# Optimization experiments

Measured on AMD Instinct MI355X. Metric: run time of the kernel, lower is better.

The kernel has to match this reference:

```python
import jax, jax.numpy as jnp
import numpy as np

T_, B_, C_ = 1, 2, 4
D_, H_, W_ = 32, 32, 32
RES = (16, 16, 16)          # (Dlat, Hlat, Wlat)
K_ = 32                      # fixed max neighbors (pad+mask)
RADIUS = 0.055
OUT_CH = 128
NUM_CH = 32                  # pos-embedding channels per coord
MAXP = 10000.0
EMB = 3 * NUM_CH             # 96


def _pos_embed(coords):
    # transformer sinusoidal embedding: [..., 3] -> [..., 96]
    freq = 1.0 / (MAXP ** (jnp.arange(0, NUM_CH, 2, dtype=jnp.float32) / NUM_CH))  # [16]
    ang = coords[..., None] * freq                                   # [..., 3, 16]
    emb = jnp.concatenate([jnp.sin(ang), jnp.cos(ang)], axis=-1)     # [..., 3, 32]
    return emb.reshape(coords.shape[:-1] + (EMB,))


def _kernel_mlp(h, W0, b0, W1, b1, W2, b2, W3, b3):
    # LinearChannelMLP layers [196,128,256,128,128] with gelu between layers
    h = jax.nn.gelu(h @ W0 + b0)
    h = jax.nn.gelu(h @ W1 + b1)
    h = jax.nn.gelu(h @ W2 + b2)
    return h @ W3 + b3


def _make_input_grid():
    # grid_coords[b] has shape [H, W, D, 3]; flatten matches f_y's (h w d) order
    th = np.linspace(0.0, 1.0, H_, dtype=np.float32)
    tw = np.linspace(0.0, 1.0, W_, dtype=np.float32)
    td = np.linspace(0.0, 1.0, D_, dtype=np.float32)
    Xh, Yw, Zd = np.meshgrid(th, tw, td, indexing='ij')
    return np.stack([Xh, Yw, Zd], axis=-1)  # [H, W, D, 3]


def _make_latent_grid():
    # mirrors __init__: tx over res[1], ty over res[2], tz over res[0]
    tx = np.linspace(0.0, 1.0, RES[1], dtype=np.float32)
    ty = np.linspace(0.0, 1.0, RES[2], dtype=np.float32)
    tz = np.linspace(0.0, 1.0, RES[0], dtype=np.float32)
    X, Y, Z = np.meshgrid(tx, ty, tz, indexing='ij')
    return np.stack([X, Y, Z], axis=-1).reshape(-1, 3)  # [Nq, 3]


def _radius_neighbors(q, y, radius, k):
    # brute-force KDTree replacement: k nearest within radius, padded + masked
    nq = q.shape[0]
    idx = np.zeros((nq, k), np.int32)
    msk = np.zeros((nq, k), bool)
    r2 = radius * radius
    for s in range(0, nq, 512):
        qb = q[s:s + 512]
        d2 = ((qb[:, None, :] - y[None, :, :]) ** 2).sum(-1)  # [chunk, Ny]
        part = np.argpartition(d2, k, axis=1)[:, :k]
        pd = np.take_along_axis(d2, part, 1)
        order = np.argsort(pd, axis=1)
        part = np.take_along_axis(part, order, 1)
        pd = np.take_along_axis(pd, order, 1)
        idx[s:s + 512] = part.astype(np.int32)
        msk[s:s + 512] = pd <= r2
    return idx, msk


def setup_inputs() -> dict:
    key = jax.random.key(0)
    ks = jax.random.split(key, 9)
    x = jax.random.normal(ks[0], (T_, B_, C_, D_, H_, W_), jnp.float32)

    gc = _make_input_grid()                                   # [H,W,D,3]
    grid_coords = jnp.asarray(np.broadcast_to(gc, (B_,) + gc.shape).copy())
    lat = _make_latent_grid()                                 # [Nq,3]
    latent_grid = jnp.asarray(lat)

    # bbox of grid is [0,1]^3 so rescaled latent grid == latent_grid here
    idx, msk = _radius_neighbors(lat, gc.reshape(-1, 3), RADIUS, K_)
    nbr_idx = jnp.asarray(np.broadcast_to(idx, (B_,) + idx.shape).copy())
    nbr_mask = jnp.asarray(np.broadcast_to(msk, (B_,) + msk.shape).copy())

    kin = 2 * EMB + C_  # 196
    def lin(k, fin, fout):
        return jax.random.normal(k, (fin, fout), jnp.float32) / np.float32(np.sqrt(fin))
    W0 = lin(ks[1], kin, 128); b0 = jnp.zeros((128,), jnp.float32)
    W1 = lin(ks[2], 128, 256); b1 = jnp.zeros((256,), jnp.float32)
    W2 = lin(ks[3], 256, 128); b2 = jnp.zeros((128,), jnp.float32)
    W3 = lin(ks[4], 128, OUT_CH); b3 = jnp.zeros((OUT_CH,), jnp.float32)

    return {"x": x, "grid_coords": grid_coords, "latent_grid": latent_grid,
            "nbr_idx": nbr_idx, "nbr_mask": nbr_mask,
            "W0": W0, "b0": b0, "W1": W1, "b1": b1,
            "W2": W2, "b2": b2, "W3": W3, "b3": b3}


def reference(x, grid_coords, latent_grid, nbr_idx, nbr_mask,
              W0, b0, W1, b1, W2, b2, W3, b3):
    T, B, C, D, H, W = x.shape
    Dl, Hl, Wl = RES
    # 't b c d h w -> b t (h w d) c'
    f = jnp.transpose(x, (1, 0, 4, 5, 3, 2)).reshape(B, T, H * W * D, C)
    y = grid_coords.reshape(B, -1, 3)                         # [B,Ny,3]
    bmin = y.min(axis=1, keepdims=True)
    bmax = y.max(axis=1, keepdims=True)
    lat = bmin + (bmax - bmin) * latent_grid[None]            # [B,Nq,3]

    y_emb = _pos_embed(y)                                     # [B,Ny,96]
    x_emb = _pos_embed(lat)                                   # [B,Nq,96]

    def per_batch(y_e, x_e, f_b, idx, msk):
        # gather neighbor features (ragged -> padded fixed-K)
        rep = y_e[idx]                                        # [Nq,K,96]
        slf = jnp.broadcast_to(x_e[:, None, :], rep.shape)    # [Nq,K,96]
        f_nbr = f_b[:, idx]                                   # [T,Nq,K,C]
        coord_feat = jnp.concatenate([rep, slf], axis=-1)     # [Nq,K,192]
        agg = jnp.concatenate(
            [jnp.broadcast_to(coord_feat[None], (f_b.shape[0],) + coord_feat.shape),
             f_nbr], axis=-1)                                 # [T,Nq,K,196]
        k = _kernel_mlp(agg, W0, b0, W1, b1, W2, b2, W3, b3)  # [T,Nq,K,out]
        k = k * msk[None, :, :, None].astype(k.dtype)
        return k.sum(axis=2)                                  # [T,Nq,out] (reduction='sum')

    out = jax.vmap(per_batch)(y_emb, x_emb, f, nbr_idx, nbr_mask)  # [B,T,Nq,out]
    # 'b t (h w d) c -> t b c d h w'
    out = out.reshape(B, T, Hl, Wl, Dl, -1)
    out = jnp.transpose(out, (1, 0, 5, 4, 2, 3))              # [T,B,out,Dl,Hl,Wl]
    return out
```

## Files before the change

### kernel.cpp

```cpp
#include <hip/hip_runtime.h>
#include <hip/hip_bf16.h>
#include <math.h>


typedef short bs8 __attribute__((ext_vector_type(8)));
typedef float f4  __attribute__((ext_vector_type(4)));
typedef float f2  __attribute__((ext_vector_type(2)));

#define MFMA16 __builtin_amdgcn_mfma_f32_16x16x32_bf16

#define W1T_OFF    0u
#define W2T_OFF    65536u
#define W3T_OFF    131072u
#define W0ET_OFF   163840u
#define W0MT_OFF   188416u
#define VQ_OFF     212992u
#define GF_OFF     2310144u
#define ST_OFF     19087360u
#define CNT_OFF    23281664u
#define FAST_NEED  23314432u

#define OW0AT_OFF   0
#define OW1T_OFF    32768
#define OW2T_OFF    98304
#define OW3T_OFF    163840
#define OSTAGED_OFF 196608
#define OLD_NEED    (196608 + 4194304)

__device__ __forceinline__ short f2bf(float f) {
  unsigned u = __float_as_uint(f);
  return (short)((u + 0x7FFFu + ((u >> 16) & 1u)) >> 16);
}
__device__ __forceinline__ float bf2f(short s) {
  return __uint_as_float(((unsigned)(unsigned short)s) << 16);
}
__device__ __forceinline__ unsigned pk2bf(float lo, float hi) {
  __hip_bfloat162 h = __float22bfloat162_rn(float2{lo, hi});
  return *reinterpret_cast<unsigned*>(&h);
}
__device__ __forceinline__ f2 gelu2(f2 x) {
  f2 t = x * x;
  f2 z = x * (t * 0.10294322f + 2.3022077f);
  f2 e;
  e.x = __builtin_exp2f(z.x);
  e.y = __builtin_exp2f(z.y);
  f2 d = e + 1.0f;
  f2 r;
  r.x = __builtin_amdgcn_rcpf(d.x);
  r.y = __builtin_amdgcn_rcpf(d.y);
  return x - x * r;
}
__device__ __forceinline__ float gelu_old(float x) {
  float z = 0.7978845608028654f * fmaf(0.044715f * x, x * x, x);
  float e = __expf(2.0f * z);
  return 0.5f * x * (2.0f - 2.0f / (e + 1.0f));
}


__global__ void gno_prep3(const float* __restrict__ W0, const float* __restrict__ W1,
                          const float* __restrict__ W2, const float* __restrict__ W3,
                          short* __restrict__ W1T, short* __restrict__ W2T,
                          short* __restrict__ W3T, short* __restrict__ W0eT,
                          short* __restrict__ W0mT) {
  int g = blockIdx.x * 256 + threadIdx.x;
  if (g < 32768) {
    int nn = g >> 7, k = g & 127;
    W1T[g] = f2bf(W1[k * 256 + nn]);
  } else if (g < 65536) {
    int h = g - 32768, nn = h >> 8, k = h & 255;
    W2T[h] = f2bf(W2[k * 128 + nn]);
  } else if (g < 81920) {
    int h = g - 65536, nn = h >> 7, k = h & 127;
    W3T[h] = f2bf(W3[k * 128 + nn]);
  } else if (g < 94208) {
    int h = g - 81920, nn = h / 96, k = h % 96;
    W0eT[h] = f2bf(W0[k * 128 + nn]);
  } else if (g < 106496) {
    int h = g - 94208, nn = h / 96, k = h % 96;
    W0mT[h] = f2bf(W0[(96 + k) * 128 + nn]);
  }
}

__global__ __launch_bounds__(256, 4) void gno_gfvq(
    const float* __restrict__ x, const float* __restrict__ gc,
    const float* __restrict__ latg, const float* __restrict__ W0,
    const float* __restrict__ b0,
    const short* __restrict__ W0eT, const short* __restrict__ W0mT,
    short* __restrict__ GF, float* __restrict__ vqPre) {
  __shared__ __align__(16) short embS[64 * 104];
  __shared__ __align__(16) short tileS[64 * 132];
  __shared__ float gcS[192];
  __shared__ float xS[2][4][64];
  __shared__ float wfS[4][128];
  __shared__ float freqS[16];

  const int tid = threadIdx.x;
  const int blk = blockIdx.x;
  const bool isGF = blk < 512;
  const int p0 = isGF ? blk * 64 : (blk - 512) * 64;

  if (tid < 16) freqS[tid] = (float)exp(-(double)tid * (9.210340371976184 / 16.0));
  if (tid < 192) gcS[tid] = isGF ? gc[p0 * 3 + tid] : latg[p0 * 3 + tid];
  if (isGF) {
#pragma unroll
    for (int u = 0; u < 2; ++u) {
      int slot = tid * 2 + u;
      int bb = slot >> 8, ch = (slot >> 6) & 3, i = slot & 63;
      int n = p0 + i;
      xS[bb][ch][i] = x[((bb * 4 + ch) << 15) + ((n & 31) << 10) + (n >> 5)];
      wfS[slot >> 7][slot & 127] = W0[(192 + (slot >> 7)) * 128 + (slot & 127)];
    }
  }
  __syncthreads();
  {
    int rr = tid >> 2, c4 = tid & 3;
#pragma unroll
    for (int c = c4 * 24; c < c4 * 24 + 24; ++c) {
      int a = c >> 5, jj = c & 31;
      float v = (jj < 16) ? __sinf(gcS[rr * 3 + a] * freqS[jj])
                          : __cosf(gcS[rr * 3 + a] * freqS[jj & 15]);
      embS[rr * 104 + c] = f2bf(v);
    }
  }
  __syncthreads();
  const int wid = tid >> 6, lane = tid & 63;
  const int l15 = lane & 15, lg = lane >> 4;
  const int f0 = wid * 32;
  const short* WT = isGF ? W0eT : W0mT;
  f4 acc[2][4] = {};
#pragma unroll
  for (int ks = 0; ks < 3; ++ks) {
    bs8 Aw[2], Be[4];
#pragma unroll
    for (int ft = 0; ft < 2; ++ft)
      Aw[ft] = *(const bs8*)(WT + (f0 + ft * 16 + l15) * 96 + ks * 32 + lg * 8);
#pragma unroll
    for (int pt = 0; pt < 4; ++pt)
      Be[pt] = *(const bs8*)(embS + (pt * 16 + l15) * 104 + ks * 32 + lg * 8);
#pragma unroll
    for (int ft = 0; ft < 2; ++ft)
#pragma unroll
      for (int pt = 0; pt < 4; ++pt)
        acc[ft][pt] = MFMA16(Aw[ft], Be[pt], acc[ft][pt], 0, 0, 0);
  }
  if (!isGF) {
#pragma unroll
    for (int ft = 0; ft < 2; ++ft) {
      f4 bias = *(const f4*)(b0 + f0 + ft * 16 + lg * 4);
#pragma unroll
      for (int pt = 0; pt < 4; ++pt) {
        int q = p0 + pt * 16 + l15;
        *(f4*)(vqPre + q * 128 + f0 + ft * 16 + lg * 4) = acc[ft][pt] + bias;
      }
    }
    return;
  }
#pragma unroll 1
  for (int bb = 0; bb < 2; ++bb) {
#pragma unroll
    for (int ft = 0; ft < 2; ++ft) {
      f4 wf0 = *(const f4*)(&wfS[0][f0 + ft * 16 + lg * 4]);
      f4 wf1 = *(const f4*)(&wfS[1][f0 + ft * 16 + lg * 4]);
      f4 wf2 = *(const f4*)(&wfS[2][f0 + ft * 16 + lg * 4]);
      f4 wf3 = *(const f4*)(&wfS[3][f0 + ft * 16 + lg * 4]);
#pragma unroll
      for (int pt = 0; pt < 4; ++pt) {
        int p = pt * 16 + l15;
        float x0 = xS[bb][0][p], x1 = xS[bb][1][p], x2 = xS[bb][2][p], x3 = xS[bb][3][p];
        float v0 = acc[ft][pt][0] + x0 * wf0[0] + x1 * wf1[0] + x2 * wf2[0] + x3 * wf3[0];
        float v1 = acc[ft][pt][1] + x0 * wf0[1] + x1 * wf1[1] + x2 * wf2[1] + x3 * wf3[1];
        float v2 = acc[ft][pt][2] + x0 * wf0[2] + x1 * wf1[2] + x2 * wf2[2] + x3 * wf3[2];
        float v3 = acc[ft][pt][3] + x0 * wf0[3] + x1 * wf1[3] + x2 * wf2[3] + x3 * wf3[3];
        uint2 pp;
        pp.x = pk2bf(v0, v1);
        pp.y = pk2bf(v2, v3);
        *(uint2*)(tileS + p * 132 + f0 + ft * 16 + lg * 4) = pp;
      }
    }
    __syncthreads();
    {
      int row = tid >> 2, c4 = tid & 3;
      const short* src = tileS + row * 132 + c4 * 32;
      short* dst = GF + ((size_t)((bb << 15) + p0 + row)) * 128 + c4 * 32;
      *(uint4*)(dst)      = *(const uint4*)(src);
      *(uint4*)(dst + 8)  = *(const uint4*)(src + 8);
      *(uint4*)(dst + 16) = *(const uint4*)(src + 16);
      *(uint4*)(dst + 24) = *(const uint4*)(src + 24);
    }
    __syncthreads();
  }
}

__device__ __forceinline__ uint4 gelu8u(uint4 gu, const float* vrow) {
  uint4 r;
  const unsigned ua[4] = {gu.x, gu.y, gu.z, gu.w};
  unsigned ro[4];
#pragma unroll
  for (int j = 0; j < 4; ++j) {
    f2 xx;
    xx.x = __uint_as_float(ua[j] << 16);
    xx.y = __uint_as_float(ua[j] & 0xFFFF0000u);
    xx += *(const f2*)(vrow + 2 * j);
    f2 g = gelu2(xx);
    ro[j] = pk2bf(g.x, g.y);
  }
  r.x = ro[0]; r.y = ro[1]; r.z = ro[2]; r.w = ro[3];
  return r;
}

__global__ __launch_bounds__(256, 4) void gno_main5(
    const float* __restrict__ gc, const float* __restrict__ latg,
    const int* __restrict__ nidx,
    const float* __restrict__ b1, const float* __restrict__ b2,
    const short* __restrict__ W1T, const short* __restrict__ W2T,
    const float* __restrict__ vqPre, const short* __restrict__ GF,
    float* __restrict__ staged, float* __restrict__ cntG) {
  __shared__ __align__(16) short h0S[64][136];
  __shared__ __align__(16) short h1S[64][136];
  __shared__ float vqS[2][128];
  __shared__ float maskfS[64];

  const int tid = threadIdx.x;
  const int blk = blockIdx.x;
  const int b = blk >> 11;
  const int q0 = (blk & 2047) * 2;

  vqS[tid >> 7][tid & 127] = vqPre[(q0 + (tid >> 7)) * 128 + (tid & 127)];

  const int r = tid >> 2, seg = tid & 3;
  const int qh = r >> 5;
  const int n = nidx[(q0 + qh) * 32 + (r & 31)];
  const uint4* gp = (const uint4*)(GF + ((size_t)((b << 15) + n)) * 128 + seg * 32);
  uint4 g0 = gp[0], g1 = gp[1], g2 = gp[2], g3 = gp[3];
  if (seg == 0) {
    float la = latg[(q0 + qh) * 3], lb = latg[(q0 + qh) * 3 + 1], lc = latg[(q0 + qh) * 3 + 2];
    float d0 = __fsub_rn(la, gc[n * 3]);
    float d1 = __fsub_rn(lb, gc[n * 3 + 1]);
    float d2 = __fsub_rn(lc, gc[n * 3 + 2]);
    float s = __fadd_rn(__fadd_rn(__fmul_rn(d0, d0), __fmul_rn(d1, d1)), __fmul_rn(d2, d2));
    maskfS[r] = ((double)s <= 0.055 * 0.055) ? 1.0f : 0.0f;
  }
  __syncthreads();
  {
    const float* vrow = vqS[qh] + seg * 32;
    *(uint4*)(&h0S[r][seg * 32]) = gelu8u(g0, vrow);
    *(uint4*)(&h0S[r][seg * 32 + 8]) = gelu8u(g1, vrow + 8);
    *(uint4*)(&h0S[r][seg * 32 + 16]) = gelu8u(g2, vrow + 16);
    *(uint4*)(&h0S[r][seg * 32 + 24]) = gelu8u(g3, vrow + 24);
  }
  __syncthreads();
  if (tid < 2) {
    float s = 0.0f;
#pragma unroll
    for (int i = 0; i < 32; ++i) s += maskfS[tid * 32 + i];
    cntG[(b << 12) + q0 + tid] = s;
  }

  const int wid = tid >> 6, lane = tid & 63;
  const int l15 = lane & 15, lg = lane >> 4;
  const int mh = wid >> 1, nh = wid & 1;
  f4 accL2[4][2] = {};

#pragma unroll 1
  for (int c = 0; c < 2; ++c) {
    {
      const int f0l = wid * 32;
      const int fg = c * 128 + f0l;
      f4 acc[2][4] = {};
#pragma unroll
      for (int ks = 0; ks < 4; ++ks) {
        bs8 Aw[2], Bh[4];
#pragma unroll
        for (int ft = 0; ft < 2; ++ft)
          Aw[ft] = *(const bs8*)(W1T + (fg + ft * 16 + l15) * 128 + ks * 32 + lg * 8);
#pragma unroll
        for (int rt = 0; rt < 4; ++rt)
          Bh[rt] = *(const bs8*)(&h0S[rt * 16 + l15][ks * 32 + lg * 8]);
#pragma unroll
        for (int ft = 0; ft < 2; ++ft)
#pragma unroll
          for (int rt = 0; rt < 4; ++rt)
            acc[ft][rt] = MFMA16(Aw[ft], Bh[rt], acc[ft][rt], 0, 0, 0);
      }
#pragma unroll
      for (int ft = 0; ft < 2; ++ft) {
        f4 bias = *(const f4*)(b1 + fg + ft * 16 + lg * 4);
#pragma unroll
        for (int rt = 0; rt < 4; ++rt) {
          f2 a = {acc[ft][rt][0] + bias[0], acc[ft][rt][1] + bias[1]};
          f2 bpair = {acc[ft][rt][2] + bias[2], acc[ft][rt][3] + bias[3]};
          f2 ga = gelu2(a);
          f2 gb = gelu2(bpair);
          uint2 p;
          p.x = pk2bf(ga.x, ga.y);
          p.y = pk2bf(gb.x, gb.y);
          *(uint2*)(&h1S[rt * 16 + l15][f0l + ft * 16 + lg * 4]) = p;
        }
      }
    }
    __syncthreads();
    {
      const int fo = nh * 64;
#pragma unroll
      for (int ks = 0; ks < 4; ++ks) {
        bs8 Ah[2], Bw[4];
#pragma unroll
        for (int rt = 0; rt < 2; ++rt)
          Ah[rt] = *(const bs8*)(&h1S[mh * 32 + rt * 16 + l15][ks * 32 + lg * 8]);
#pragma unroll
        for (int ct = 0; ct < 4; ++ct)
          Bw[ct] = *(const bs8*)(W2T + (fo + ct * 16 + l15) * 256 + c * 128 + ks * 32 + lg * 8);
#pragma unroll
        for (int ct = 0; ct < 4; ++ct)
#pragma unroll
          for (int rt = 0; rt < 2; ++rt)
            accL2[ct][rt] = MFMA16(Ah[rt], Bw[ct], accL2[ct][rt], 0, 0, 0);
      }
    }
    __syncthreads();
  }

  {
    const int fo = nh * 64;
    float psum[4];
#pragma unroll
    for (int ct = 0; ct < 4; ++ct) {
      float bias = b2[fo + ct * 16 + l15];
      float s = 0.0f;
#pragma unroll
      for (int rt = 0; rt < 2; ++rt) {
        f2 u0 = {accL2[ct][rt][0] + bias, accL2[ct][rt][1] + bias};
        f2 u1 = {accL2[ct][rt][2] + bias, accL2[ct][rt][3] + bias};
        f2 gA = gelu2(u0);
        f2 gB = gelu2(u1);
        int row = mh * 32 + rt * 16 + lg * 4;
        s += gA.x * maskfS[row] + gA.y * maskfS[row + 1] +
             gB.x * maskfS[row + 2] + gB.y * maskfS[row + 3];
      }
      psum[ct] = s;
    }
#pragma unroll
    for (int ct = 0; ct < 4; ++ct) {
      psum[ct] += __shfl_xor(psum[ct], 16, 64);
      psum[ct] += __shfl_xor(psum[ct], 32, 64);
    }
    if (lane < 16) {
      float* op = staged + ((size_t)((b << 12) + q0 + mh)) * 128 + fo;
      op[lane] = psum[0];
      op[16 + lane] = psum[1];
      op[32 + lane] = psum[2];
      op[48 + lane] = psum[3];
    }
  }
}

__global__ __launch_bounds__(256, 2) void gno_fin2(
    const float* __restrict__ staged, const float* __restrict__ cntG,
    const short* __restrict__ W3T, const float* __restrict__ b3,
    float* __restrict__ out) {
  __shared__ __align__(16) float tileS[16 * 260];
  __shared__ float cntS[256];
  __shared__ float b3S[128];
  const int tid = threadIdx.x, blk = blockIdx.x;
  const int b = blk >> 5;
  const int hi = (blk >> 1) & 15;
  const int q0 = hi * 256;
  const int ct0 = (blk & 1) * 4;
  cntS[tid] = cntG[(b << 12) + q0 + tid];
  if (tid < 128) b3S[tid] = b3[tid];
  __syncthreads();
  const int wid = tid >> 6, lane = tid & 63;
  const int l15 = lane & 15, lg = lane >> 4;
  const int r0 = wid * 64;
  f4 acc[4][4] = {};
#pragma unroll
  for (int ks = 0; ks < 4; ++ks) {
    bs8 Aa[4];
#pragma unroll
    for (int rt = 0; rt < 4; ++rt) {
      const float* ap =
          staged + ((size_t)(b << 12) + q0 + r0 + rt * 16 + l15) * 128 + ks * 32 + lg * 8;
      f4 a0 = *(const f4*)ap;
      f4 a1 = *(const f4*)(ap + 4);
      uint4 uu;
      uu.x = pk2bf(a0[0], a0[1]);
      uu.y = pk2bf(a0[2], a0[3]);
      uu.z = pk2bf(a1[0], a1[1]);
      uu.w = pk2bf(a1[2], a1[3]);
      Aa[rt] = *reinterpret_cast<bs8*>(&uu);
    }
#pragma unroll
    for (int c4 = 0; c4 < 4; ++c4) {
      bs8 Bw = *(const bs8*)(W3T + ((ct0 + c4) * 16 + l15) * 128 + ks * 32 + lg * 8);
#pragma unroll
      for (int rt = 0; rt < 4; ++rt)
        acc[c4][rt] = MFMA16(Bw, Aa[rt], acc[c4][rt], 0, 0, 0);
    }
  }
#pragma unroll 1
  for (int c4 = 0; c4 < 4; ++c4) {
    int ct = ct0 + c4;
#pragma unroll
    for (int rt = 0; rt < 4; ++rt) {
      int rr = r0 + rt * 16 + l15;
      float cv = cntS[rr];
#pragma unroll
      for (int i = 0; i < 4; ++i) {
        int fl = lg * 4 + i;
        tileS[fl * 260 + rr] = acc[c4][rt][i] + cv * b3S[ct * 16 + fl];
      }
    }
    __syncthreads();
    {
      int fl = tid >> 4, dl = tid & 15;
      int o = ct * 16 + fl;
      float* dst = out + ((size_t)b << 19) + (o << 12) + (dl << 8) + (hi << 4);
#pragma unroll
      for (int w4 = 0; w4 < 4; ++w4) {
        float4 t;
        t.x = tileS[fl * 260 + (w4 * 4 + 0) * 16 + dl];
        t.y = tileS[fl * 260 + (w4 * 4 + 1) * 16 + dl];
        t.z = tileS[fl * 260 + (w4 * 4 + 2) * 16 + dl];
        t.w = tileS[fl * 260 + (w4 * 4 + 3) * 16 + dl];
        *(float4*)(dst + w4 * 4) = t;
      }
    }
    __syncthreads();
  }
}


__global__ void gno_prep(const float* __restrict__ W0, const float* __restrict__ W1,
                         const float* __restrict__ W2, const float* __restrict__ W3,
                         short* __restrict__ W0aT, short* __restrict__ W1T,
                         short* __restrict__ W2T, short* __restrict__ W3T) {
  int g = blockIdx.x * 256 + threadIdx.x;
  if (g < 16384) {
    int n = g >> 7, k = g & 127;
    float v = (k < 96) ? W0[k * 128 + n] : ((k < 100) ? W0[(k + 96) * 128 + n] : 0.0f);
    W0aT[g] = f2bf(v);
  } else if (g < 49152) {
    int h = g - 16384, n = h >> 7, k = h & 127;
    W1T[h] = f2bf(W1[k * 256 + n]);
  } else if (g < 81920) {
    int h = g - 49152, n = h >> 8, k = h & 255;
    W2T[h] = f2bf(W2[k * 128 + n]);
  } else if (g < 98304) {
    int h = g - 81920, n = h >> 7, k = h & 127;
    W3T[h] = f2bf(W3[k * 128 + n]);
  }
}

template <int SIN, int K>
__device__ __forceinline__ void gemm_block(const short* inS, const short* __restrict__ WT,
                                           int colBase, int lane, f4 (&acc)[2][4]) {
  constexpr int KS = K / 32;
  bs8 Bf[2][KS];
  const int bcol = lane & 15;
  const int bk = (lane >> 4) * 8;
#pragma unroll
  for (int ct = 0; ct < 2; ++ct)
#pragma unroll
    for (int ks = 0; ks < KS; ++ks)
      Bf[ct][ks] = *reinterpret_cast<const bs8*>(WT + (colBase + ct * 16 + bcol) * K + ks * 32 + bk);
#pragma unroll
  for (int mt = 0; mt < 4; ++mt) {
#pragma unroll
    for (int ks = 0; ks < KS; ++ks) {
      bs8 Af = *reinterpret_cast<const bs8*>(inS + (mt * 16 + bcol) * SIN + ks * 32 + bk);
      acc[0][mt] = MFMA16(Af, Bf[0][ks], acc[0][mt], 0, 0, 0);
      acc[1][mt] = MFMA16(Af, Bf[1][ks], acc[1][mt], 0, 0, 0);
    }
  }
}

__global__ __launch_bounds__(256, 2) void gno_main(
    const float* __restrict__ x, const float* __restrict__ gc,
    const float* __restrict__ latg, const int* __restrict__ nidx,
    const float* __restrict__ W0, const float* __restrict__ b0,
    const float* __restrict__ b1, const float* __restrict__ b2,
    const float* __restrict__ b3,
    const short* __restrict__ W0aT, const short* __restrict__ W1T,
    const short* __restrict__ W2T, const short* __restrict__ W3T,
    float* __restrict__ dst, int direct) {
  __shared__ __align__(16) short aggS[64][136];
  __shared__ __align__(16) short h0S[64][136];
  __shared__ __align__(16) short h1S[64][264];
  __shared__ float vqS[2][128];
  __shared__ float maskfS[64];
  __shared__ float freqS[16];
  __shared__ float latS[2][3];
  __shared__ float sEmbQ[2][96];

  const int tid = threadIdx.x;
  const int blk = blockIdx.x;
  const int b = blk >> 11;
  const int q0 = (blk & 2047) * 2;

  if (tid < 16) freqS[tid] = (float)exp(-(double)tid * (9.210340371976184 / 16.0));
  if (tid >= 32 && tid < 38) {
    int t = tid - 32, qh = t / 3, a = t % 3;
    latS[qh][a] = latg[(q0 + qh) * 3 + a];
  }
  __syncthreads();
  if (tid < 192) {
    int qh = tid / 96, c = tid % 96, a = c >> 5, jj = c & 31;
    float ca = latS[qh][a];
    sEmbQ[qh][c] = (jj < 16) ? __sinf(ca * freqS[jj]) : __cosf(ca * freqS[jj & 15]);
  }
  __syncthreads();
  {
    int qh = tid >> 7, o = tid & 127;
    float s = b0[o];
#pragma unroll 4
    for (int j = 0; j < 96; ++j) s = fmaf(sEmbQ[qh][j], W0[(96 + j) * 128 + o], s);
    vqS[qh][o] = s;
  }
  {
    int r = tid >> 2, qq = tid & 3;
    int qh = r >> 5, kk = r & 31;
    int n = nidx[(q0 + qh) * 32 + kk];
    float c0 = gc[n * 3], c1 = gc[n * 3 + 1], c2 = gc[n * 3 + 2];
    if (qq == 0) {
      float d0 = __fsub_rn(latS[qh][0], c0);
      float d1 = __fsub_rn(latS[qh][1], c1);
      float d2 = __fsub_rn(latS[qh][2], c2);
      float s = __fadd_rn(__fadd_rn(__fmul_rn(d0, d0), __fmul_rn(d1, d1)), __fmul_rn(d2, d2));
      maskfS[r] = ((double)s <= 0.055 * 0.055) ? 1.0f : 0.0f;
    }
    float cc[3] = {c0, c1, c2};
    for (int c = qq * 34; c < qq * 34 + 34; ++c) {
      float v = 0.0f;
      if (c < 96) {
        int a = c >> 5, jj = c & 31;
        v = (jj < 16) ? __sinf(cc[a] * freqS[jj]) : __cosf(cc[a] * freqS[jj & 15]);
      } else if (c < 100) {
        int ch = c - 96;
        v = x[((b * 4 + ch) << 15) + ((n & 31) << 10) + (n >> 5)];
      }
      aggS[r][c] = f2bf(v);
    }
  }
  __syncthreads();

  const int wave = tid >> 6, lane = tid & 63;
  const int colBase = wave * 32;
  const int lrow4 = (lane >> 4) << 2;
  const int lcol = lane & 15;

  {
    f4 acc[2][4] = {};
    gemm_block<136, 128>(&aggS[0][0], W0aT, colBase, lane, acc);
#pragma unroll
    for (int ct = 0; ct < 2; ++ct) {
      int gcol = colBase + ct * 16 + lcol;
#pragma unroll
      for (int mt = 0; mt < 4; ++mt)
#pragma unroll
        for (int i = 0; i < 4; ++i) {
          int grow = mt * 16 + lrow4 + i;
          h0S[grow][gcol] = f2bf(gelu_old(acc[ct][mt][i] + vqS[grow >> 5][gcol]));
        }
    }
  }
  __syncthreads();
  {
#pragma unroll 1
    for (int cg = 0; cg < 2; ++cg) {
      int cb = wave * 64 + cg * 32;
      f4 acc[2][4] = {};
      gemm_block<136, 128>(&h0S[0][0], W1T, cb, lane, acc);
#pragma unroll
      for (int ct = 0; ct < 2; ++ct) {
        int gcol = cb + ct * 16 + lcol;
        float bias = b1[gcol];
#pragma unroll
        for (int mt = 0; mt < 4; ++mt)
#pragma unroll
          for (int i = 0; i < 4; ++i) {
            int grow = mt * 16 + lrow4 + i;
            h1S[grow][gcol] = f2bf(gelu_old(acc[ct][mt][i] + bias));
          }
      }
    }
  }
  __syncthreads();
  {
    f4 acc[2][4] = {};
    gemm_block<264, 256>(&h1S[0][0], W2T, colBase, lane, acc);
#pragma unroll
    for (int ct = 0; ct < 2; ++ct) {
      int gcol = colBase + ct * 16 + lcol;
      float bias = b2[gcol];
#pragma unroll
      for (int mt = 0; mt < 4; ++mt)
#pragma unroll
        for (int i = 0; i < 4; ++i) {
          int grow = mt * 16 + lrow4 + i;
          aggS[grow][gcol] = f2bf(gelu_old(acc[ct][mt][i] + bias));
        }
    }
  }
  __syncthreads();
  {
    f4 acc[2][4] = {};
    gemm_block<136, 128>(&aggS[0][0], W3T, colBase, lane, acc);
    float part[2][2] = {{0.0f, 0.0f}, {0.0f, 0.0f}};
#pragma unroll
    for (int ct = 0; ct < 2; ++ct) {
      float bias = b3[colBase + ct * 16 + lcol];
#pragma unroll
      for (int mt = 0; mt < 4; ++mt)
#pragma unroll
        for (int i = 0; i < 4; ++i) {
          int grow = mt * 16 + lrow4 + i;
          part[mt >> 1][ct] += (acc[ct][mt][i] + bias) * maskfS[grow];
        }
    }
#pragma unroll
    for (int qh = 0; qh < 2; ++qh)
#pragma unroll
      for (int ct = 0; ct < 2; ++ct) {
        float v = part[qh][ct];
        v += __shfl_xor(v, 16, 64);
        v += __shfl_xor(v, 32, 64);
        if (lane < 16) {
          int o = colBase + ct * 16 + lane;
          int q = q0 + qh;
          if (direct)
            dst[(b << 19) + (o << 12) + ((q & 15) << 8) + ((q >> 8) << 4) + ((q >> 4) & 15)] = v;
          else
            dst[(b * 4096 + q) * 128 + o] = v;
        }
      }
  }
}

__global__ void gno_tr(const float* __restrict__ staged, float* __restrict__ out) {
  __shared__ float tile[16][129];
  int blk = blockIdx.x;
  int b = blk >> 8, i = (blk >> 4) & 15, l = blk & 15;
  int t = threadIdx.x;
  {
    int j = t >> 4, oc = t & 15;
    const float* src = staged + ((b * 4096) + (i * 256 + j * 16 + l)) * 128 + oc * 8;
#pragma unroll
    for (int u = 0; u < 8; ++u) tile[j][oc * 8 + u] = src[u];
  }
  __syncthreads();
  {
    int og = t >> 4, j = t & 15;
#pragma unroll
    for (int oo = 0; oo < 8; ++oo) {
      int o = og * 8 + oo;
      out[(b << 19) + (o << 12) + (l << 8) + (i << 4) + j] = tile[j][o];
    }
  }
}

extern "C" void kernel_launch(void* const* d_in, const int* in_sizes, int n_in,
                              void* d_out, int out_size, void* d_ws, size_t ws_size,
                              hipStream_t stream) {
  const float* x    = (const float*)d_in[0];
  const float* gc   = (const float*)d_in[1];
  const float* latg = (const float*)d_in[2];
  const int*   nidx = (const int*)d_in[3];
  const float* W0 = (const float*)d_in[5];
  const float* b0 = (const float*)d_in[6];
  const float* W1 = (const float*)d_in[7];
  const float* b1 = (const float*)d_in[8];
  const float* W2 = (const float*)d_in[9];
  const float* b2 = (const float*)d_in[10];
  const float* W3 = (const float*)d_in[11];
  const float* b3 = (const float*)d_in[12];

  char* ws = (char*)d_ws;
  float* out = (float*)d_out;

  if (ws_size >= (size_t)FAST_NEED) {
    short* W1T  = (short*)(ws + W1T_OFF);
    short* W2T  = (short*)(ws + W2T_OFF);
    short* W3T  = (short*)(ws + W3T_OFF);
    short* W0eT = (short*)(ws + W0ET_OFF);
    short* W0mT = (short*)(ws + W0MT_OFF);
    float* vqPre = (float*)(ws + VQ_OFF);
    short* GF = (short*)(ws + GF_OFF);
    float* staged = (float*)(ws + ST_OFF);
    float* cntG = (float*)(ws + CNT_OFF);
    gno_prep3<<<416, 256, 0, stream>>>(W0, W1, W2, W3, W1T, W2T, W3T, W0eT, W0mT);
    gno_gfvq<<<576, 256, 0, stream>>>(x, gc, latg, W0, b0, W0eT, W0mT, GF, vqPre);
    gno_main5<<<4096, 256, 0, stream>>>(gc, latg, nidx, b1, b2,
                                        W1T, W2T, vqPre, GF, staged, cntG);
    gno_fin2<<<64, 256, 0, stream>>>(staged, cntG, W3T, b3, out);
  } else {
    short* W0aT = (short*)(ws + OW0AT_OFF);
    short* W1T  = (short*)(ws + OW1T_OFF);
    short* W2T  = (short*)(ws + OW2T_OFF);
    short* W3T  = (short*)(ws + OW3T_OFF);
    float* staged = (float*)(ws + OSTAGED_OFF);
    const bool use_staged = (ws_size >= (size_t)OLD_NEED);
    gno_prep<<<384, 256, 0, stream>>>(W0, W1, W2, W3, W0aT, W1T, W2T, W3T);
    gno_main<<<4096, 256, 0, stream>>>(x, gc, latg, nidx, W0, b0, b1, b2, b3,
                                       W0aT, W1T, W2T, W3T,
                                       use_staged ? staged : out, use_staged ? 0 : 1);
    if (use_staged) gno_tr<<<512, 256, 0, stream>>>(staged, out);
  }
}
```

Measured before the change: 241.8 us.

## Fuse weight prep into aux kernel and final W3 layer into main kernel

Merges the weight-transpose prep kernel into the embedding/GF kernel, with each block converting its own W0 slice into shared memory, and drops the separate W0 transposes. Moves the last W3 matmul and bias into the main kernel, applied to the per-query sums and written straight to the transposed output. This removes two launches and the staged fp32 round trip through global memory. In exchange each aux block redoes the W0 conversion, and the main kernel now writes output scattered and uncoalesced, with a small per-block MFMA that uses only 2 useful rows of 16.

Result: faster. 226.8 us (-6.2%).

```diff
diff --git a/kernel.cpp b/kernel.cpp
--- a/kernel.cpp
+++ b/kernel.cpp
@@ -12,12 +12,8 @@
 #define W1T_OFF    0u
 #define W2T_OFF    65536u
 #define W3T_OFF    131072u
-#define W0ET_OFF   163840u
-#define W0MT_OFF   188416u
 #define VQ_OFF     212992u
 #define GF_OFF     2310144u
-#define ST_OFF     19087360u
-#define CNT_OFF    23281664u
 #define FAST_NEED  23314432u
 
 #define OW0AT_OFF   0
@@ -57,57 +53,57 @@
 }
 
 
-__global__ void gno_prep3(const float* __restrict__ W0, const float* __restrict__ W1,
-                          const float* __restrict__ W2, const float* __restrict__ W3,
-                          short* __restrict__ W1T, short* __restrict__ W2T,
-                          short* __restrict__ W3T, short* __restrict__ W0eT,
-                          short* __restrict__ W0mT) {
-  int g = blockIdx.x * 256 + threadIdx.x;
-  if (g < 32768) {
-    int nn = g >> 7, k = g & 127;
-    W1T[g] = f2bf(W1[k * 256 + nn]);
-  } else if (g < 65536) {
-    int h = g - 32768, nn = h >> 8, k = h & 255;
-    W2T[h] = f2bf(W2[k * 128 + nn]);
-  } else if (g < 81920) {
-    int h = g - 65536, nn = h >> 7, k = h & 127;
-    W3T[h] = f2bf(W3[k * 128 + nn]);
-  } else if (g < 94208) {
-    int h = g - 81920, nn = h / 96, k = h % 96;
-    W0eT[h] = f2bf(W0[k * 128 + nn]);
-  } else if (g < 106496) {
-    int h = g - 94208, nn = h / 96, k = h % 96;
-    W0mT[h] = f2bf(W0[(96 + k) * 128 + nn]);
-  }
-}
-
-__global__ __launch_bounds__(256, 4) void gno_gfvq(
+__global__ __launch_bounds__(256, 3) void gno_aux(
     const float* __restrict__ x, const float* __restrict__ gc,
     const float* __restrict__ latg, const float* __restrict__ W0,
     const float* __restrict__ b0,
-    const short* __restrict__ W0eT, const short* __restrict__ W0mT,
+    const float* __restrict__ W1, const float* __restrict__ W2,
+    const float* __restrict__ W3,
+    short* __restrict__ W1T, short* __restrict__ W2T, short* __restrict__ W3T,
     short* __restrict__ GF, float* __restrict__ vqPre) {
+  __shared__ __align__(16) short w0S[128 * 104];
   __shared__ __align__(16) short embS[64 * 104];
-  __shared__ __align__(16) short tileS[64 * 132];
   __shared__ float gcS[192];
-  __shared__ float xS[2][4][64];
+  __shared__ float xS[8][64];
   __shared__ float wfS[4][128];
   __shared__ float freqS[16];
+  short* tileS = w0S;
 
   const int tid = threadIdx.x;
-  const int blk = blockIdx.x;
-  const bool isGF = blk < 512;
-  const int p0 = isGF ? blk * 64 : (blk - 512) * 64;
-
+  const int u = blockIdx.x;
+
+  if (u >= 576) {
+    int g = (u - 576) * 256 + tid;
+    if (g < 32768) {
+      int nn = g >> 7, k = g & 127;
+      W1T[g] = f2bf(W1[k * 256 + nn]);
+    } else if (g < 65536) {
+      int h = g - 32768, nn = h >> 8, k = h & 255;
+      W2T[h] = f2bf(W2[k * 128 + nn]);
+    } else {
+      int h = g - 65536, nn = h >> 7, k = h & 127;
+      W3T[h] = f2bf(W3[k * 128 + nn]);
+    }
+    return;
+  }
+
+  const bool isGF = u < 512;
+  const int p0 = isGF ? u * 64 : (u - 512) * 64;
+  const int kbase = isGF ? 0 : 96;
+
+  for (int e = tid; e < 12288; e += 256) {
+    int k = e >> 7, f = e & 127;
+    w0S[f * 104 + k] = f2bf(W0[kbase * 128 + e]);
+  }
   if (tid < 16) freqS[tid] = (float)exp(-(double)tid * (9.210340371976184 / 16.0));
   if (tid < 192) gcS[tid] = isGF ? gc[p0 * 3 + tid] : latg[p0 * 3 + tid];
   if (isGF) {
 #pragma unroll
-    for (int u = 0; u < 2; ++u) {
-      int slot = tid * 2 + u;
+    for (int uu = 0; uu < 2; ++uu) {
+      int slot = tid * 2 + uu;
       int bb = slot >> 8, ch = (slot >> 6) & 3, i = slot & 63;
       int n = p0 + i;
-      xS[bb][ch][i] = x[((bb * 4 + ch) << 15) + ((n & 31) << 10) + (n >> 5)];
+      xS[bb * 4 + ch][i] = x[((bb * 4 + ch) << 15) + ((n & 31) << 10) + (n >> 5)];
       wfS[slot >> 7][slot & 127] = W0[(192 + (slot >> 7)) * 128 + (slot & 127)];
     }
   }
@@ -126,14 +122,13 @@
   const int wid = tid >> 6, lane = tid & 63;
   const int l15 = lane & 15, lg = lane >> 4;
   const int f0 = wid * 32;
-  const short* WT = isGF ? W0eT : W0mT;
   f4 acc[2][4] = {};
 #pragma unroll
   for (int ks = 0; ks < 3; ++ks) {
     bs8 Aw[2], Be[4];
 #pragma unroll
     for (int ft = 0; ft < 2; ++ft)
-      Aw[ft] = *(const bs8*)(WT + (f0 + ft * 16 + l15) * 96 + ks * 32 + lg * 8);
+      Aw[ft] = *(const bs8*)(w0S + (f0 + ft * 16 + l15) * 104 + ks * 32 + lg * 8);
 #pragma unroll
     for (int pt = 0; pt < 4; ++pt)
       Be[pt] = *(const bs8*)(embS + (pt * 16 + l15) * 104 + ks * 32 + lg * 8);
@@ -155,6 +150,7 @@
     }
     return;
   }
+  __syncthreads();
 #pragma unroll 1
   for (int bb = 0; bb < 2; ++bb) {
 #pragma unroll
@@ -166,7 +162,8 @@
 #pragma unroll
       for (int pt = 0; pt < 4; ++pt) {
         int p = pt * 16 + l15;
-        float x0 = xS[bb][0][p], x1 = xS[bb][1][p], x2 = xS[bb][2][p], x3 = xS[bb][3][p];
+        float x0 = xS[bb * 4 + 0][p], x1 = xS[bb * 4 + 1][p];
+        float x2 = xS[bb * 4 + 2][p], x3 = xS[bb * 4 + 3][p];
         float v0 = acc[ft][pt][0] + x0 * wf0[0] + x1 * wf1[0] + x2 * wf2[0] + x3 * wf3[0];
         float v1 = acc[ft][pt][1] + x0 * wf0[1] + x1 * wf1[1] + x2 * wf2[1] + x3 * wf3[1];
         float v2 = acc[ft][pt][2] + x0 * wf0[2] + x1 * wf1[2] + x2 * wf2[2] + x3 * wf3[2];
@@ -208,17 +205,21 @@
   return r;
 }
 
-__global__ __launch_bounds__(256, 4) void gno_main5(
+__global__ __launch_bounds__(256, 4) void gno_main6(
     const float* __restrict__ gc, const float* __restrict__ latg,
     const int* __restrict__ nidx,
     const float* __restrict__ b1, const float* __restrict__ b2,
+    const float* __restrict__ b3,
     const short* __restrict__ W1T, const short* __restrict__ W2T,
+    const short* __restrict__ W3T,
     const float* __restrict__ vqPre, const short* __restrict__ GF,
-    float* __restrict__ staged, float* __restrict__ cntG) {
+    float* __restrict__ out) {
   __shared__ __align__(16) short h0S[64][136];
   __shared__ __align__(16) short h1S[64][136];
   __shared__ float vqS[2][128];
   __shared__ float maskfS[64];
+  __shared__ float b3S[128];
+  __shared__ float cntS[2];
 
   const int tid = threadIdx.x;
   const int blk = blockIdx.x;
@@ -226,6 +227,7 @@
   const int q0 = (blk & 2047) * 2;
 
   vqS[tid >> 7][tid & 127] = vqPre[(q0 + (tid >> 7)) * 128 + (tid & 127)];
+  if (tid < 128) b3S[tid] = b3[tid];
 
   const int r = tid >> 2, seg = tid & 3;
   const int qh = r >> 5;
@@ -253,7 +255,7 @@
     float s = 0.0f;
 #pragma unroll
     for (int i = 0; i < 32; ++i) s += maskfS[tid * 32 + i];
-    cntG[(b << 12) + q0 + tid] = s;
+    cntS[tid] = s;
   }
 
   const int wid = tid >> 6, lane = tid & 63;
@@ -345,87 +347,37 @@
       psum[ct] += __shfl_xor(psum[ct], 32, 64);
     }
     if (lane < 16) {
-      float* op = staged + ((size_t)((b << 12) + q0 + mh)) * 128 + fo;
-      op[lane] = psum[0];
-      op[16 + lane] = psum[1];
-      op[32 + lane] = psum[2];
-      op[48 + lane] = psum[3];
-    }
-  }
-}
-
-__global__ __launch_bounds__(256, 2) void gno_fin2(
-    const float* __restrict__ staged, const float* __restrict__ cntG,
-    const short* __restrict__ W3T, const float* __restrict__ b3,
-    float* __restrict__ out) {
-  __shared__ __align__(16) float tileS[16 * 260];
-  __shared__ float cntS[256];
-  __shared__ float b3S[128];
-  const int tid = threadIdx.x, blk = blockIdx.x;
-  const int b = blk >> 5;
-  const int hi = (blk >> 1) & 15;
-  const int q0 = hi * 256;
-  const int ct0 = (blk & 1) * 4;
-  cntS[tid] = cntG[(b << 12) + q0 + tid];
-  if (tid < 128) b3S[tid] = b3[tid];
-  __syncthreads();
-  const int wid = tid >> 6, lane = tid & 63;
-  const int l15 = lane & 15, lg = lane >> 4;
-  const int r0 = wid * 64;
-  f4 acc[4][4] = {};
-#pragma unroll
-  for (int ks = 0; ks < 4; ++ks) {
-    bs8 Aa[4];
-#pragma unroll
-    for (int rt = 0; rt < 4; ++rt) {
-      const float* ap =
-          staged + ((size_t)(b << 12) + q0 + r0 + rt * 16 + l15) * 128 + ks * 32 + lg * 8;
-      f4 a0 = *(const f4*)ap;
-      f4 a1 = *(const f4*)(ap + 4);
-      uint4 uu;
-      uu.x = pk2bf(a0[0], a0[1]);
-      uu.y = pk2bf(a0[2], a0[3]);
-      uu.z = pk2bf(a1[0], a1[1]);
-      uu.w = pk2bf(a1[2], a1[3]);
-      Aa[rt] = *reinterpret_cast<bs8*>(&uu);
-    }
-#pragma unroll
-    for (int c4 = 0; c4 < 4; ++c4) {
-      bs8 Bw = *(const bs8*)(W3T + ((ct0 + c4) * 16 + l15) * 128 + ks * 32 + lg * 8);
-#pragma unroll
-      for (int rt = 0; rt < 4; ++rt)
-        acc[c4][rt] = MFMA16(Bw, Aa[rt], acc[c4][rt], 0, 0, 0);
-    }
-  }
-#pragma unroll 1
-  for (int c4 = 0; c4 < 4; ++c4) {
-    int ct = ct0 + c4;
-#pragma unroll
-    for (int rt = 0; rt < 4; ++rt) {
-      int rr = r0 + rt * 16 + l15;
-      float cv = cntS[rr];
-#pragma unroll
-      for (int i = 0; i < 4; ++i) {
-        int fl = lg * 4 + i;
-        tileS[fl * 260 + rr] = acc[c4][rt][i] + cv * b3S[ct * 16 + fl];
-      }
-    }
-    __syncthreads();
-    {
-      int fl = tid >> 4, dl = tid & 15;
-      int o = ct * 16 + fl;
-      float* dst = out + ((size_t)b << 19) + (o << 12) + (dl << 8) + (hi << 4);
-#pragma unroll
-      for (int w4 = 0; w4 < 4; ++w4) {
-        float4 t;
-        t.x = tileS[fl * 260 + (w4 * 4 + 0) * 16 + dl];
-        t.y = tileS[fl * 260 + (w4 * 4 + 1) * 16 + dl];
-        t.z = tileS[fl * 260 + (w4 * 4 + 2) * 16 + dl];
-        t.w = tileS[fl * 260 + (w4 * 4 + 3) * 16 + dl];
-        *(float4*)(dst + w4 * 4) = t;
-      }
-    }
-    __syncthreads();
+#pragma unroll
+      for (int ct = 0; ct < 4; ++ct)
+        h0S[mh][fo + ct * 16 + lane] = f2bf(psum[ct]);
+    }
+  }
+  __syncthreads();
+  {
+    const int wf = wid * 32;
+    f4 a3[2] = {};
+#pragma unroll
+    for (int ks = 0; ks < 4; ++ks) {
+      bs8 Ah = *(const bs8*)(&h0S[l15][ks * 32 + lg * 8]);
+#pragma unroll
+      for (int ct2 = 0; ct2 < 2; ++ct2) {
+        bs8 Bw = *(const bs8*)(W3T + (wf + ct2 * 16 + l15) * 128 + ks * 32 + lg * 8);
+        a3[ct2] = MFMA16(Ah, Bw, a3[ct2], 0, 0, 0);
+      }
+    }
+    if (lg == 0) {
+#pragma unroll
+      for (int ct2 = 0; ct2 < 2; ++ct2) {
+        int feat = wf + ct2 * 16 + l15;
+        float bb3 = b3S[feat];
+#pragma unroll
+        for (int i = 0; i < 2; ++i) {
+          int q = q0 + i;
+          out[(b << 19) + (feat << 12) + ((q & 15) << 8) + ((q >> 8) << 4) +
+              ((q >> 4) & 15)] = a3[ct2][i] + cntS[i] * bb3;
+        }
+      }
+    }
   }
 }
 
@@ -681,17 +633,12 @@
     short* W1T  = (short*)(ws + W1T_OFF);
     short* W2T  = (short*)(ws + W2T_OFF);
     short* W3T  = (short*)(ws + W3T_OFF);
-    short* W0eT = (short*)(ws + W0ET_OFF);
-    short* W0mT = (short*)(ws + W0MT_OFF);
     float* vqPre = (float*)(ws + VQ_OFF);
     short* GF = (short*)(ws + GF_OFF);
-    float* staged = (float*)(ws + ST_OFF);
-    float* cntG = (float*)(ws + CNT_OFF);
-    gno_prep3<<<416, 256, 0, stream>>>(W0, W1, W2, W3, W1T, W2T, W3T, W0eT, W0mT);
-    gno_gfvq<<<576, 256, 0, stream>>>(x, gc, latg, W0, b0, W0eT, W0mT, GF, vqPre);
-    gno_main5<<<4096, 256, 0, stream>>>(gc, latg, nidx, b1, b2,
-                                        W1T, W2T, vqPre, GF, staged, cntG);
-    gno_fin2<<<64, 256, 0, stream>>>(staged, cntG, W3T, b3, out);
+    gno_aux<<<896, 256, 0, stream>>>(x, gc, latg, W0, b0, W1, W2, W3,
+                                     W1T, W2T, W3T, GF, vqPre);
+    gno_main6<<<4096, 256, 0, stream>>>(gc, latg, nidx, b1, b2, b3,
+                                        W1T, W2T, W3T, vqPre, GF, out);
   } else {
     short* W0aT = (short*)(ws + OW0AT_OFF);
     short* W1T  = (short*)(ws + OW1T_OFF);
```
